# Kernel tuning notes

Hardware: AMD Instinct MI355X
Metric: run time of the kernel (lower is better)

## Reference

```python
import jax, jax.numpy as jnp
import numpy as np

B, NAV, H, W = 16, 36, 120, 160
HID, AEMB, NF = 512, 32, 4

def _conv(x, w, b, stride, pad, dil, groups):
    y = jax.lax.conv_general_dilated(x, w, stride, pad, rhs_dilation=dil, feature_group_count=groups)
    return y + b[None, :, None, None]

def _avgpool(x, k, s):
    y = jax.lax.reduce_window(x, 0.0, jax.lax.add, (1, 1) + k, (1, 1) + s, 'VALID')
    return y / float(k[0] * k[1])

def _conv2_block(x, w1, b1, w2, b2):
    # conv2_1: k5 stride (5,7) dilation 10 -> avgpool 3/3 -> conv2_2: k3 stride 2 dilation (1,2) -> avgpool (3,9)/3
    y = _conv(x, w1, b1, (5, 7), ((0, 0), (0, 0)), (10, 10), 1)
    y = _avgpool(y, (3, 3), (3, 3))
    y = _conv(y, w2, b2, (2, 2), ((0, 0), (0, 0)), (1, 2), 1)
    y = _avgpool(y, (3, 9), (3, 3))
    return y[:, 0]  # [B,3,12]

def setup_inputs() -> dict:
    key = jax.random.key(0)
    ks = jax.random.split(key, 24)
    s = 0.02
    d = {}
    d['depth_feat_0'] = jax.random.normal(ks[0], (B, NAV, H, W), jnp.float32)
    d['depth_feat_1'] = jax.random.normal(ks[1], (B, NAV, H, W), jnp.float32)
    d['obj_detection_feat'] = jax.random.normal(ks[2], (B, NAV, H, W), jnp.float32)
    d['num_navigable_feat'] = jax.random.uniform(ks[3], (B, NAV), jnp.float32)
    d['pre_action_feat'] = jax.random.normal(ks[4], (B, AEMB), jnp.float32)
    d['h_0'] = jax.random.normal(ks[5], (B, HID), jnp.float32)
    d['c_0'] = jax.random.normal(ks[6], (B, HID), jnp.float32)
    d['weighted_ctx'] = jax.random.normal(ks[7], (B, HID), jnp.float32)
    d['navigable_index'] = jax.random.randint(ks[8], (B, 8), 0, NAV).astype(jnp.int32)
    # params
    d['conv1_w'] = jax.random.normal(ks[9], (NAV, 2, 5, 5), jnp.float32) * s
    d['conv1_b'] = jnp.zeros((NAV,), jnp.float32)
    d['dyn_filters'] = jax.random.normal(ks[10], (NF, NAV, 2, 5, 5), jnp.float32) * s
    d['dyn_w1'] = jax.random.normal(ks[11], (HID, HID // 4), jnp.float32) * s
    d['dyn_b1'] = jnp.zeros((HID // 4,), jnp.float32)
    d['dyn_w2'] = jax.random.normal(ks[12], (HID // 4, NF), jnp.float32) * s
    d['dyn_b2'] = jnp.zeros((NF,), jnp.float32)
    d['conv2_1_w'] = jax.random.normal(ks[13], (1, 1, 5, 5), jnp.float32) * s
    d['conv2_1_b'] = jnp.zeros((1,), jnp.float32)
    d['conv2_2_w'] = jax.random.normal(ks[14], (1, 1, 3, 3), jnp.float32) * s
    d['conv2_2_b'] = jnp.zeros((1,), jnp.float32)
    in_sz = HID + NAV + NF + AEMB  # 584
    d['lstm_w_ih'] = jax.random.normal(ks[15], (4 * HID, in_sz), jnp.float32) * s
    d['lstm_w_hh'] = jax.random.normal(ks[16], (4 * HID, HID), jnp.float32) * s
    d['lstm_b_ih'] = jnp.zeros((4 * HID,), jnp.float32)
    d['lstm_b_hh'] = jnp.zeros((4 * HID,), jnp.float32)
    return d

def reference(depth_feat_0, depth_feat_1, obj_detection_feat, num_navigable_feat, pre_action_feat, h_0, c_0, weighted_ctx, navigable_index, conv1_w, conv1_b, dyn_filters, dyn_w1, dyn_b1, dyn_w2, dyn_b2, conv2_1_w, conv2_1_b, conv2_2_w, conv2_2_b, lstm_w_ih, lstm_w_hh, lstm_b_ih, lstm_b_hh):
    Bv = depth_feat_0.shape[0]
    # interleave depth channels: [B,72,H,W] (replaces 36-iter python copy loop)
    mid1 = jnp.stack([depth_feat_0, depth_feat_1], axis=2).reshape(Bv, 2 * NAV, H, W)
    total_depth = _conv(mid1, conv1_w, conv1_b, (1, 1), ((2, 2), (2, 2)), (1, 1), NAV)  # [B,36,H,W]
    nav_attn = jax.nn.softmax(num_navigable_feat, axis=1)[:, :, None, None]
    mid2 = jnp.stack([total_depth * nav_attn, obj_detection_feat * nav_attn], axis=2).reshape(Bv, 2 * NAV, H, W)
    # dynamic conv: per-sample filter = attention-weighted mix of NF learned grouped filters
    filt_attn = jax.nn.softmax(jax.nn.relu(weighted_ctx @ dyn_w1 + dyn_b1) @ dyn_w2 + dyn_b2, axis=1)  # [B,4]
    kern = jnp.einsum('bf,fgikl->bgikl', filt_attn, dyn_filters).reshape(Bv * NAV, 2, 5, 5)
    dyn_out = jax.lax.conv_general_dilated(mid2.reshape(1, Bv * 2 * NAV, H, W), kern, (1, 1), ((2, 2), (2, 2)), feature_group_count=Bv * NAV).reshape(Bv, NAV, H, W)
    # panorama canvas assembly: tile i -> row block (2 - i//12), col i%12
    canvas = dyn_out.reshape(Bv, 3, 12, H, W)[:, ::-1].transpose(0, 1, 3, 2, 4).reshape(Bv, 1, 3 * H, 12 * W)
    v1 = _conv2_block(canvas, conv2_1_w, conv2_1_b, conv2_2_w, conv2_2_b)
    rolled = jnp.concatenate([canvas[..., -W:], canvas[..., :-W]], axis=-1)
    v2 = _conv2_block(rolled, conv2_1_w, conv2_1_b, conv2_2_w, conv2_2_b)
    v2 = jnp.concatenate([v2[:, :, 1:], v2[:, :, :1]], axis=-1)
    vf = ((v1 + v2) * 0.5)[:, ::-1].reshape(Bv, NAV)  # flip row dim then flatten
    vf = jax.nn.softmax(vf / 10.0, axis=1)  # self.softmax_temperature hardcoded to 10
    concat = jnp.concatenate([weighted_ctx, vf, filt_attn, pre_action_feat], axis=1)
    gates = concat @ lstm_w_ih.T + lstm_b_ih + h_0 @ lstm_w_hh.T + lstm_b_hh
    i, f, g, o = jnp.split(gates, 4, axis=1)
    c_1 = jax.nn.sigmoid(f) * c_0 + jax.nn.sigmoid(i) * jnp.tanh(g)
    h_1 = jax.nn.sigmoid(o) * jnp.tanh(c_1)
    mask = jnp.zeros((Bv, NAV + 1), jnp.float32).at[:, 0].set(1.0)
    mask = mask.at[jnp.arange(Bv)[:, None], navigable_index + 1].set(1.0)
    return (h_1, c_1, vf, mask)
```

## Files before the change

### kernel.cpp

```cpp
#include <hip/hip_runtime.h>
#include <math.h>

#define B_ 16
#define NAV_ 36
#define H_ 120
#define W_ 160
#define HID_ 512
#define PLANES (B_*NAV_)
#define PLANE_PX (H_*W_)
#define CANVAS_H 360
#define CANVAS_W 1920
#define CANVAS_PX (CANVAS_H*CANVAS_W)

#define OUT_H 12
#define ST_ROWS 16
#define ROWB 352
#define CHSTR (ST_ROWS*ROWB)

#define WS_NAV    0
#define WS_FATT   576
#define WS_KERN   640
#define WS_TD     29440
#define WS_CANVAS (WS_TD + PLANES*PLANE_PX)
#define WS_POOL1  (WS_CANVAS + B_*CANVAS_PX)
#define WS_VF     (WS_POOL1 + B_*2*19*89)

typedef unsigned int u32;
typedef _Float16 h2_t __attribute__((ext_vector_type(2)));
typedef float float4a __attribute__((ext_vector_type(4), aligned(4)));

__device__ __forceinline__ float sigmoidf_(float x) { return 1.f / (1.f + expf(-x)); }

__device__ __forceinline__ u32 pkh(float a, float b) {
    return __builtin_bit_cast(u32, __builtin_amdgcn_cvt_pkrtz(a, b));
}
__device__ __forceinline__ float dot2h(u32 a, u32 b, float c) {
#if __has_builtin(__builtin_amdgcn_fdot2)
    return __builtin_amdgcn_fdot2(__builtin_bit_cast(h2_t, a),
                                  __builtin_bit_cast(h2_t, b), c, false);
#else
    float r;
    asm("v_dot2_f32_f16 %0, %1, %2, %3" : "=v"(r) : "v"(a), "v"(b), "v"(c));
    return r;
#endif
}

__device__ __forceinline__ void stage2(unsigned char* lds, const float* s0,
                                       const float* s1, int r0, int tid)
{
    for (int i = tid; i < 2*ST_ROWS*44; i += 256) {
        const int ch  = i / (ST_ROWS*44);
        const int rem = i % (ST_ROWS*44);
        const int rr  = rem / 44;
        const int j   = rem % 44;
        const int gr  = r0 - 2 + rr;
        u32 lo = 0, hi = 0;
        if ((unsigned)gr < (unsigned)H_ && j <= 40) {
            const float* src = (ch ? s1 : s0) + gr*W_;
            if (j == 0) {
                hi = pkh(src[0], src[1]);
            } else if (j < 40) {
                const float4a v = *(const float4a*)(src + 4*j - 2);
                lo = pkh(v.x, v.y);  hi = pkh(v.z, v.w);
            } else {
                lo = pkh(src[158], src[159]);
            }
        }
        *(int2*)(lds + (size_t)ch*CHSTR + rr*ROWB + j*8) = make_int2((int)lo, (int)hi);
    }
}

__device__ __forceinline__ void conv8(const unsigned char* b0, const unsigned char* b1,
                                      const u32* ew, float* acc)
{
    #pragma unroll
    for (int ky = 0; ky < 5; ++ky) {
        const int off = ky*ROWB;
        int4 qa = *(const int4*)(b0 + off);
        int2 qb = *(const int2*)(b0 + off + 16);
        int4 ra = *(const int4*)(b1 + off);
        int2 rb = *(const int2*)(b1 + off + 16);
        u32 P[6] = {(u32)qa.x,(u32)qa.y,(u32)qa.z,(u32)qa.w,(u32)qb.x,(u32)qb.y};
        u32 Q[6] = {(u32)ra.x,(u32)ra.y,(u32)ra.z,(u32)ra.w,(u32)rb.x,(u32)rb.y};
        const u32 e0 = ew[ky*3+0], e1 = ew[ky*3+1], e2 = ew[ky*3+2];
        const u32 f0 = ew[15+ky*3+0], f1 = ew[15+ky*3+1], f2 = ew[15+ky*3+2];
        const u32 o0 = e0 << 16;
        const u32 o1 = __builtin_amdgcn_alignbit(e1, e0, 16);
        const u32 o2 = __builtin_amdgcn_alignbit(e2, e1, 16);
        const u32 g0 = f0 << 16;
        const u32 g1 = __builtin_amdgcn_alignbit(f1, f0, 16);
        const u32 g2 = __builtin_amdgcn_alignbit(f2, f1, 16);
        #pragma unroll
        for (int m = 0; m < 4; ++m) {
            acc[2*m]   = dot2h(e0, P[m], dot2h(e1, P[m+1], dot2h(e2, P[m+2], acc[2*m])));
            acc[2*m+1] = dot2h(o0, P[m], dot2h(o1, P[m+1], dot2h(o2, P[m+2], acc[2*m+1])));
            acc[2*m]   = dot2h(f0, Q[m], dot2h(f1, Q[m+1], dot2h(f2, Q[m+2], acc[2*m])));
            acc[2*m+1] = dot2h(g0, Q[m], dot2h(g1, Q[m+1], dot2h(g2, Q[m+2], acc[2*m+1])));
        }
    }
}

#define LOAD_EW(EW, SW)                                                        \
    {                                                                          \
        _Pragma("unroll")                                                      \
        for (int q = 0; q < 7; ++q) {                                          \
            int4 t = ((const int4*)(SW))[q];                                   \
            EW[4*q]=(u32)t.x; EW[4*q+1]=(u32)t.y; EW[4*q+2]=(u32)t.z; EW[4*q+3]=(u32)t.w; \
        }                                                                      \
        int2 t = ((const int2*)(SW))[14];                                      \
        EW[28]=(u32)t.x; EW[29]=(u32)t.y;                                      \
    }

__global__ __launch_bounds__(256)
void k_td(const float* __restrict__ d0, const float* __restrict__ d1,
          const float* __restrict__ conv1_w, const float* __restrict__ conv1_b,
          const float* __restrict__ wctx, const float* __restrict__ dw1,
          const float* __restrict__ db1, const float* __restrict__ dw2,
          const float* __restrict__ db2, const float* __restrict__ dynf,
          const float* __restrict__ numnav, float* __restrict__ ws)
{
    const int tid = threadIdx.x;
    const int plane = blockIdx.y;

    __shared__ __align__(16) unsigned char smem[2*CHSTR + 160];
    u32* swt2 = (u32*)(smem + 2*CHSTR);
    float* sextra = (float*)(swt2 + 32);

    if (blockIdx.x == 10) {
        if (plane % NAV_) return;
        const int b = plane / NAV_;
        float* sh   = (float*)smem;
        float* sred = sh + 128;
        float* nv   = sh + 136;
        float* nms  = sh + 172;
        if (tid < 128) {
            float acc = db1[tid];
            for (int k = 0; k < HID_; ++k) acc += wctx[b*HID_ + k] * dw1[k*128 + tid];
            sh[tid] = fmaxf(acc, 0.f);
        }
        __syncthreads();
        if (tid < 4) {
            float acc = db2[tid];
            for (int j = 0; j < 128; ++j) acc += sh[j] * dw2[j*4 + tid];
            sred[tid] = acc;
        }
        __syncthreads();
        if (tid == 0) {
            float m = fmaxf(fmaxf(sred[0], sred[1]), fmaxf(sred[2], sred[3]));
            float e0 = expf(sred[0]-m), e1 = expf(sred[1]-m), e2 = expf(sred[2]-m), e3 = expf(sred[3]-m);
            float s = e0+e1+e2+e3;
            sred[4] = e0/s; sred[5] = e1/s; sred[6] = e2/s; sred[7] = e3/s;
            ws[WS_FATT + b*4+0] = sred[4]; ws[WS_FATT + b*4+1] = sred[5];
            ws[WS_FATT + b*4+2] = sred[6]; ws[WS_FATT + b*4+3] = sred[7];
        }
        __syncthreads();
        {
            const float fa0 = sred[4], fa1 = sred[5], fa2 = sred[6], fa3 = sred[7];
            for (int e = tid; e < 1800; e += 256) {
                float v = fa0*dynf[e] + fa1*dynf[1800+e] + fa2*dynf[3600+e] + fa3*dynf[5400+e];
                ws[WS_KERN + b*1800 + e] = v;
            }
        }
        if (tid < 36) nv[tid] = numnav[b*NAV_ + tid];
        __syncthreads();
        if (tid == 0) {
            float m = nv[0];
            for (int i = 1; i < 36; ++i) m = fmaxf(m, nv[i]);
            float s = 0.f;
            for (int i = 0; i < 36; ++i) s += expf(nv[i]-m);
            nms[0] = m; nms[1] = s;
        }
        __syncthreads();
        if (tid < 36) ws[WS_NAV + b*NAV_ + tid] = expf(nv[tid]-nms[0]) / nms[1];
        return;
    }

    const int g = plane % NAV_;
    const int r0 = blockIdx.x * OUT_H;

    if (tid < 30) {
        const int ch = tid / 15, ky = (tid % 15) / 3, k = tid % 3;
        const float* wsrc = conv1_w + g*50 + ch*25 + ky*5;
        const float a0 = wsrc[2*k];
        const float a1 = (k < 2) ? wsrc[2*k+1] : 0.f;
        swt2[tid] = pkh(a0, a1);
    }
    if (tid == 30) sextra[0] = conv1_b[g];

    stage2(smem, d0 + (size_t)plane*PLANE_PX, d1 + (size_t)plane*PLANE_PX, r0, tid);
    __syncthreads();

    if (tid < 240) {
        const int yr = tid / 20, s = tid % 20;
        const unsigned char* b0 = smem + yr*ROWB + s*16;
        const unsigned char* b1 = b0 + CHSTR;
        float acc[8];
        #pragma unroll
        for (int p = 0; p < 8; ++p) acc[p] = 0.f;
        u32 ew[30];
        LOAD_EW(ew, swt2)
        conv8(b0, b1, ew, acc);
        const float bias = sextra[0];
        float* outp = ws + WS_TD + (size_t)plane*PLANE_PX + (r0+yr)*W_ + s*8;
        *(float4*)outp     = make_float4(acc[0]+bias, acc[1]+bias, acc[2]+bias, acc[3]+bias);
        *(float4*)(outp+4) = make_float4(acc[4]+bias, acc[5]+bias, acc[6]+bias, acc[7]+bias);
    }
}

__global__ __launch_bounds__(256)
void k_dyn(const float* __restrict__ obj, float* __restrict__ ws)
{
    const int tid = threadIdx.x;
    const int plane = blockIdx.y;
    const int b = plane / NAV_;
    const int g = plane % NAV_;
    const int r0 = blockIdx.x * OUT_H;

    __shared__ __align__(16) unsigned char smem[2*CHSTR + 160];
    u32* swt2 = (u32*)(smem + 2*CHSTR);
    float* sextra = (float*)(swt2 + 32);

    if (tid < 30) {
        const int ch = tid / 15, ky = (tid % 15) / 3, k = tid % 3;
        const float* wsrc = ws + WS_KERN + plane*50 + ch*25 + ky*5;
        const float a0 = wsrc[2*k];
        const float a1 = (k < 2) ? wsrc[2*k+1] : 0.f;
        swt2[tid] = pkh(a0, a1);
    }
    if (tid == 30) sextra[0] = ws[WS_NAV + plane];

    stage2(smem, ws + WS_TD + (size_t)plane*PLANE_PX,
           obj + (size_t)plane*PLANE_PX, r0, tid);
    __syncthreads();

    if (tid < 240) {
        const int yr = tid / 20, s = tid % 20;
        const unsigned char* b0 = smem + yr*ROWB + s*16;
        const unsigned char* b1 = b0 + CHSTR;
        float acc[8];
        #pragma unroll
        for (int p = 0; p < 8; ++p) acc[p] = 0.f;
        u32 ew[30];
        LOAD_EW(ew, swt2)
        conv8(b0, b1, ew, acc);
        const float a = sextra[0];
        const int rowblk = 2 - g/12;
        const int colblk = g % 12;
        float* cbase = ws + WS_CANVAS + (size_t)b*CANVAS_PX
                     + (size_t)(rowblk*H_ + r0 + yr)*CANVAS_W + colblk*W_ + s*8;
        *(float4*)cbase     = make_float4(a*acc[0], a*acc[1], a*acc[2], a*acc[3]);
        *(float4*)(cbase+4) = make_float4(a*acc[4], a*acc[5], a*acc[6], a*acc[7]);
    }
}

__global__ __launch_bounds__(256)
void k_conv2a(const float* __restrict__ w21p, const float* __restrict__ b21p,
              float* __restrict__ ws)
{
    const int blk = blockIdx.x;
    const int a = blk % 19;
    const int bv = blk / 19;
    const int ver = bv & 1;
    const int b = bv >> 1;
    const int coloff = ver ? (CANVAS_W - W_) : 0;

    __shared__ float s1[3*267];
    __shared__ float swt[25];
    if (threadIdx.x < 25) swt[threadIdx.x] = w21p[threadIdx.x];
    __syncthreads();
    const float b21 = b21p[0];
    const float* cv = ws + WS_CANVAS + (size_t)b*CANVAS_PX;

    for (int px = threadIdx.x; px < 3*267; px += 256) {
        const int row = px / 267;
        const int v = px % 267;
        const int u = 3*a + row;
        float acc = b21;
        #pragma unroll
        for (int ky = 0; ky < 5; ++ky) {
            const float* rp = cv + (5*u + 10*ky)*CANVAS_W;
            #pragma unroll
            for (int kx = 0; kx < 5; ++kx) {
                int c = 7*v + 10*kx + coloff;
                if (c >= CANVAS_W) c -= CANVAS_W;
                acc += swt[ky*5+kx] * rp[c];
            }
        }
        s1[px] = acc;
    }
    __syncthreads();
    if (threadIdx.x < 89) {
        const int bb = threadIdx.x;
        float s = 0.f;
        #pragma unroll
        for (int i = 0; i < 3; ++i)
            #pragma unroll
            for (int j = 0; j < 3; ++j)
                s += s1[i*267 + 3*bb + j];
        ws[WS_POOL1 + blk*89 + bb] = s * (1.f/9.f);
    }
}

__global__ __launch_bounds__(256)
void k_conv2b(const float* __restrict__ w22p, const float* __restrict__ b22p,
              const int* __restrict__ navidx, float* __restrict__ ws,
              float* __restrict__ out)
{
    const int b = blockIdx.x;
    __shared__ float p[2*19*89];
    __shared__ float s2[2*9*43];
    __shared__ float svf[36];
    __shared__ float sms[2];
    __shared__ float swt[9];

    for (int i = threadIdx.x; i < 2*19*89; i += 256)
        p[i] = ws[WS_POOL1 + (b*2)*19*89 + i];
    if (threadIdx.x < 9) swt[threadIdx.x] = w22p[threadIdx.x];
    const float b22 = b22p[0];
    __syncthreads();

    for (int t = threadIdx.x; t < 2*9*43; t += 256) {
        const int ver = t / 387;
        const int r = t % 387;
        const int pp = r / 43;
        const int q = r % 43;
        float acc = b22;
        #pragma unroll
        for (int i = 0; i < 3; ++i)
            #pragma unroll
            for (int j = 0; j < 3; ++j)
                acc += swt[i*3+j] * p[(ver*19 + (2*pp+i))*89 + 2*q + 2*j];
        s2[ver*387 + pp*43 + q] = acc;
    }
    __syncthreads();

    if (threadIdx.x < 36) {
        const int gg = threadIdx.x;
        const int io = 2 - gg/12;
        const int j  = gg % 12;
        const int j2 = (j + 1) % 12;
        float s = 0.f;
        #pragma unroll
        for (int ii = 0; ii < 3; ++ii)
            #pragma unroll
            for (int jj = 0; jj < 9; ++jj)
                s += s2[(3*io+ii)*43 + 3*j + jj] + s2[387 + (3*io+ii)*43 + 3*j2 + jj];
        svf[gg] = s * (0.5f/27.f);
    }
    __syncthreads();
    if (threadIdx.x == 0) {
        float m = svf[0];
        for (int i = 1; i < 36; ++i) m = fmaxf(m, svf[i]);
        float s = 0.f;
        for (int i = 0; i < 36; ++i) s += expf((svf[i]-m)*0.1f);
        sms[0] = m; sms[1] = s;
    }
    __syncthreads();
    if (threadIdx.x < 36) {
        const float v = expf((svf[threadIdx.x]-sms[0])*0.1f) / sms[1];
        ws[WS_VF + b*36 + threadIdx.x] = v;
        out[16384 + b*36 + threadIdx.x] = v;
    }
    if (threadIdx.x < 37) {
        const int j = threadIdx.x;
        float v = (j == 0) ? 1.f : 0.f;
        #pragma unroll
        for (int t = 0; t < 8; ++t)
            if (navidx[b*8+t] + 1 == j) v = 1.f;
        out[16960 + b*37 + j] = v;
    }
}

#define CT_STRIDE 20
__global__ __launch_bounds__(256)
void k_lstm(const float* __restrict__ wctx, const float* __restrict__ pre_action,
            const float* __restrict__ h0, const float* __restrict__ c0,
            const float* __restrict__ w_ih, const float* __restrict__ w_hh,
            const float* __restrict__ b_ih, const float* __restrict__ b_hh,
            const float* __restrict__ ws, float* __restrict__ out)
{
    __shared__ float cT[1096*CT_STRIDE];
    __shared__ float red[8*32*16];
    __shared__ float gatev[8][16];
    const int tid = threadIdx.x;

    for (int idx = tid; idx < 1096*16; idx += 256) {
        const int k = idx >> 4;
        const int bb = idx & 15;
        float v;
        if (k < 512)       v = wctx[bb*512 + k];
        else if (k < 548)  v = ws[WS_VF + bb*36 + (k-512)];
        else if (k < 552)  v = ws[WS_FATT + bb*4 + (k-548)];
        else if (k < 584)  v = pre_action[bb*32 + (k-552)];
        else               v = h0[bb*512 + (k-584)];
        cT[k*CT_STRIDE + bb] = v;
    }
    __syncthreads();

    const int rl = tid >> 5;
    const int lane = tid & 31;
    const int u0 = blockIdx.x*2;
    const int ul = rl & 1;
    const int gate = rl >> 1;
    const int r = u0 + ul + gate*512;

    float acc[16];
    #pragma unroll
    for (int i = 0; i < 16; ++i) acc[i] = 0.f;

    const float* wih_r = w_ih + (size_t)r*584;
    for (int k = lane; k < 584; k += 32) {
        const float wv = wih_r[k];
        const float* cp = cT + k*CT_STRIDE;
        #pragma unroll
        for (int i = 0; i < 16; ++i) acc[i] += wv*cp[i];
    }
    const float* whh_r = w_hh + (size_t)r*512;
    for (int k = lane; k < 512; k += 32) {
        const float wv = whh_r[k];
        const float* cp = cT + (584+k)*CT_STRIDE;
        #pragma unroll
        for (int i = 0; i < 16; ++i) acc[i] += wv*cp[i];
    }
    float* rp = red + (rl*32 + lane)*16;
    #pragma unroll
    for (int i = 0; i < 16; ++i) rp[i] = acc[i];
    __syncthreads();

    if (tid < 128) {
        const int rr = tid >> 4;
        const int bb = tid & 15;
        const int rrow = u0 + (rr & 1) + (rr >> 1)*512;
        float s = b_ih[rrow] + b_hh[rrow];
        for (int l = 0; l < 32; ++l) s += red[(rr*32 + l)*16 + bb];
        gatev[rr][bb] = s;
    }
    __syncthreads();

    if (tid < 32) {
        const int ul2 = tid >> 4;
        const int bb = tid & 15;
        const int u = u0 + ul2;
        const float gi = gatev[0+ul2][bb];
        const float gf = gatev[2+ul2][bb];
        const float gg = gatev[4+ul2][bb];
        const float go = gatev[6+ul2][bb];
        const float c1 = sigmoidf_(gf)*c0[bb*512+u] + sigmoidf_(gi)*tanhf(gg);
        const float h1 = sigmoidf_(go)*tanhf(c1);
        out[bb*512 + u] = h1;
        out[8192 + bb*512 + u] = c1;
    }
}

extern "C" void kernel_launch(void* const* d_in, const int* in_sizes, int n_in,
                              void* d_out, int out_size, void* d_ws, size_t ws_size,
                              hipStream_t stream)
{
    const float* d0        = (const float*)d_in[0];
    const float* d1        = (const float*)d_in[1];
    const float* obj       = (const float*)d_in[2];
    const float* numnav    = (const float*)d_in[3];
    const float* preact    = (const float*)d_in[4];
    const float* h0        = (const float*)d_in[5];
    const float* c0        = (const float*)d_in[6];
    const float* wctx      = (const float*)d_in[7];
    const int*   navidx    = (const int*)d_in[8];
    const float* conv1_w   = (const float*)d_in[9];
    const float* conv1_b   = (const float*)d_in[10];
    const float* dynf      = (const float*)d_in[11];
    const float* dw1       = (const float*)d_in[12];
    const float* db1       = (const float*)d_in[13];
    const float* dw2       = (const float*)d_in[14];
    const float* db2       = (const float*)d_in[15];
    const float* w21       = (const float*)d_in[16];
    const float* b21       = (const float*)d_in[17];
    const float* w22       = (const float*)d_in[18];
    const float* b22       = (const float*)d_in[19];
    const float* wih       = (const float*)d_in[20];
    const float* whh       = (const float*)d_in[21];
    const float* bih       = (const float*)d_in[22];
    const float* bhh       = (const float*)d_in[23];
    float* ws  = (float*)d_ws;
    float* out = (float*)d_out;

    dim3 blk(256);
    k_td    <<<dim3(11, 576), blk, 0, stream>>>(d0, d1, conv1_w, conv1_b, wctx,
                                                dw1, db1, dw2, db2, dynf, numnav, ws);
    k_dyn   <<<dim3(10, 576), blk, 0, stream>>>(obj, ws);
    k_conv2a<<<dim3(608),     blk, 0, stream>>>(w21, b21, ws);
    k_conv2b<<<dim3(16),      blk, 0, stream>>>(w22, b22, navidx, ws, out);
    k_lstm  <<<dim3(256),     blk, 0, stream>>>(wctx, preact, h0, c0, wih, whh,
                                                bih, bhh, ws, out);
}
```

Before: 146.0 us.

## Fuse depth conv and dynamic conv into one kernel with halo recompute in LDS

```diff
diff --git a/kernel.cpp b/kernel.cpp
--- a/kernel.cpp
+++ b/kernel.cpp
@@ -13,9 +13,11 @@
 #define CANVAS_PX (CANVAS_H*CANVAS_W)
 
 #define OUT_H 12
-#define ST_ROWS 16
+#define IN_ROWS 20
+#define TD_ROWS 16
+#define OBJ_ROWS 16
 #define ROWB 352
-#define CHSTR (ST_ROWS*ROWB)
+#define INCH (IN_ROWS*ROWB)
 
 #define WS_NAV    0
 #define WS_FATT   576
@@ -43,31 +45,6 @@
     asm("v_dot2_f32_f16 %0, %1, %2, %3" : "=v"(r) : "v"(a), "v"(b), "v"(c));
     return r;
 #endif
-}
-
-__device__ __forceinline__ void stage2(unsigned char* lds, const float* s0,
-                                       const float* s1, int r0, int tid)
-{
-    for (int i = tid; i < 2*ST_ROWS*44; i += 256) {
-        const int ch  = i / (ST_ROWS*44);
-        const int rem = i % (ST_ROWS*44);
-        const int rr  = rem / 44;
-        const int j   = rem % 44;
-        const int gr  = r0 - 2 + rr;
-        u32 lo = 0, hi = 0;
-        if ((unsigned)gr < (unsigned)H_ && j <= 40) {
-            const float* src = (ch ? s1 : s0) + gr*W_;
-            if (j == 0) {
-                hi = pkh(src[0], src[1]);
-            } else if (j < 40) {
-                const float4a v = *(const float4a*)(src + 4*j - 2);
-                lo = pkh(v.x, v.y);  hi = pkh(v.z, v.w);
-            } else {
-                lo = pkh(src[158], src[159]);
-            }
-        }
-        *(int2*)(lds + (size_t)ch*CHSTR + rr*ROWB + j*8) = make_int2((int)lo, (int)hi);
-    }
 }
 
 __device__ __forceinline__ void conv8(const unsigned char* b0, const unsigned char* b1,
@@ -104,146 +81,164 @@
     {                                                                          \
         _Pragma("unroll")                                                      \
         for (int q = 0; q < 7; ++q) {                                          \
-            int4 t = ((const int4*)(SW))[q];                                   \
-            EW[4*q]=(u32)t.x; EW[4*q+1]=(u32)t.y; EW[4*q+2]=(u32)t.z; EW[4*q+3]=(u32)t.w; \
+            int4 t_ = ((const int4*)(SW))[q];                                  \
+            EW[4*q]=(u32)t_.x; EW[4*q+1]=(u32)t_.y; EW[4*q+2]=(u32)t_.z; EW[4*q+3]=(u32)t_.w; \
         }                                                                      \
-        int2 t = ((const int2*)(SW))[14];                                      \
-        EW[28]=(u32)t.x; EW[29]=(u32)t.y;                                      \
+        int2 t_ = ((const int2*)(SW))[14];                                     \
+        EW[28]=(u32)t_.x; EW[29]=(u32)t_.y;                                    \
     }
 
 __global__ __launch_bounds__(256)
-void k_td(const float* __restrict__ d0, const float* __restrict__ d1,
-          const float* __restrict__ conv1_w, const float* __restrict__ conv1_b,
-          const float* __restrict__ wctx, const float* __restrict__ dw1,
-          const float* __restrict__ db1, const float* __restrict__ dw2,
-          const float* __restrict__ db2, const float* __restrict__ dynf,
-          const float* __restrict__ numnav, float* __restrict__ ws)
+void k_pre(const float* __restrict__ wctx, const float* __restrict__ dw1,
+           const float* __restrict__ db1, const float* __restrict__ dw2,
+           const float* __restrict__ db2, const float* __restrict__ dynf,
+           const float* __restrict__ numnav, float* __restrict__ ws)
 {
     const int tid = threadIdx.x;
-    const int plane = blockIdx.y;
-
-    __shared__ __align__(16) unsigned char smem[2*CHSTR + 160];
-    u32* swt2 = (u32*)(smem + 2*CHSTR);
-    float* sextra = (float*)(swt2 + 32);
-
-    if (blockIdx.x == 10) {
-        if (plane % NAV_) return;
-        const int b = plane / NAV_;
-        float* sh   = (float*)smem;
-        float* sred = sh + 128;
-        float* nv   = sh + 136;
-        float* nms  = sh + 172;
-        if (tid < 128) {
-            float acc = db1[tid];
-            for (int k = 0; k < HID_; ++k) acc += wctx[b*HID_ + k] * dw1[k*128 + tid];
-            sh[tid] = fmaxf(acc, 0.f);
-        }
-        __syncthreads();
-        if (tid < 4) {
-            float acc = db2[tid];
-            for (int j = 0; j < 128; ++j) acc += sh[j] * dw2[j*4 + tid];
-            sred[tid] = acc;
-        }
-        __syncthreads();
-        if (tid == 0) {
-            float m = fmaxf(fmaxf(sred[0], sred[1]), fmaxf(sred[2], sred[3]));
-            float e0 = expf(sred[0]-m), e1 = expf(sred[1]-m), e2 = expf(sred[2]-m), e3 = expf(sred[3]-m);
-            float s = e0+e1+e2+e3;
-            sred[4] = e0/s; sred[5] = e1/s; sred[6] = e2/s; sred[7] = e3/s;
-            ws[WS_FATT + b*4+0] = sred[4]; ws[WS_FATT + b*4+1] = sred[5];
-            ws[WS_FATT + b*4+2] = sred[6]; ws[WS_FATT + b*4+3] = sred[7];
-        }
-        __syncthreads();
-        {
-            const float fa0 = sred[4], fa1 = sred[5], fa2 = sred[6], fa3 = sred[7];
-            for (int e = tid; e < 1800; e += 256) {
-                float v = fa0*dynf[e] + fa1*dynf[1800+e] + fa2*dynf[3600+e] + fa3*dynf[5400+e];
-                ws[WS_KERN + b*1800 + e] = v;
-            }
-        }
-        if (tid < 36) nv[tid] = numnav[b*NAV_ + tid];
-        __syncthreads();
-        if (tid == 0) {
-            float m = nv[0];
-            for (int i = 1; i < 36; ++i) m = fmaxf(m, nv[i]);
-            float s = 0.f;
-            for (int i = 0; i < 36; ++i) s += expf(nv[i]-m);
-            nms[0] = m; nms[1] = s;
-        }
-        __syncthreads();
-        if (tid < 36) ws[WS_NAV + b*NAV_ + tid] = expf(nv[tid]-nms[0]) / nms[1];
-        return;
-    }
-
-    const int g = plane % NAV_;
-    const int r0 = blockIdx.x * OUT_H;
-
-    if (tid < 30) {
-        const int ch = tid / 15, ky = (tid % 15) / 3, k = tid % 3;
-        const float* wsrc = conv1_w + g*50 + ch*25 + ky*5;
-        const float a0 = wsrc[2*k];
-        const float a1 = (k < 2) ? wsrc[2*k+1] : 0.f;
-        swt2[tid] = pkh(a0, a1);
-    }
-    if (tid == 30) sextra[0] = conv1_b[g];
-
-    stage2(smem, d0 + (size_t)plane*PLANE_PX, d1 + (size_t)plane*PLANE_PX, r0, tid);
-    __syncthreads();
-
-    if (tid < 240) {
-        const int yr = tid / 20, s = tid % 20;
-        const unsigned char* b0 = smem + yr*ROWB + s*16;
-        const unsigned char* b1 = b0 + CHSTR;
-        float acc[8];
-        #pragma unroll
-        for (int p = 0; p < 8; ++p) acc[p] = 0.f;
-        u32 ew[30];
-        LOAD_EW(ew, swt2)
-        conv8(b0, b1, ew, acc);
-        const float bias = sextra[0];
-        float* outp = ws + WS_TD + (size_t)plane*PLANE_PX + (r0+yr)*W_ + s*8;
-        *(float4*)outp     = make_float4(acc[0]+bias, acc[1]+bias, acc[2]+bias, acc[3]+bias);
-        *(float4*)(outp+4) = make_float4(acc[4]+bias, acc[5]+bias, acc[6]+bias, acc[7]+bias);
-    }
+    const int b = blockIdx.x;
+    __shared__ float sh[128];
+    __shared__ float sred[8];
+    __shared__ float nv[36];
+    __shared__ float nms[2];
+    if (tid < 128) {
+        float acc = db1[tid];
+        for (int k = 0; k < HID_; ++k) acc += wctx[b*HID_ + k] * dw1[k*128 + tid];
+        sh[tid] = fmaxf(acc, 0.f);
+    }
+    __syncthreads();
+    if (tid < 4) {
+        float acc = db2[tid];
+        for (int j = 0; j < 128; ++j) acc += sh[j] * dw2[j*4 + tid];
+        sred[tid] = acc;
+    }
+    __syncthreads();
+    if (tid == 0) {
+        float m = fmaxf(fmaxf(sred[0], sred[1]), fmaxf(sred[2], sred[3]));
+        float e0 = expf(sred[0]-m), e1 = expf(sred[1]-m), e2 = expf(sred[2]-m), e3 = expf(sred[3]-m);
+        float s = e0+e1+e2+e3;
+        sred[4] = e0/s; sred[5] = e1/s; sred[6] = e2/s; sred[7] = e3/s;
+        ws[WS_FATT + b*4+0] = sred[4]; ws[WS_FATT + b*4+1] = sred[5];
+        ws[WS_FATT + b*4+2] = sred[6]; ws[WS_FATT + b*4+3] = sred[7];
+    }
+    __syncthreads();
+    {
+        const float fa0 = sred[4], fa1 = sred[5], fa2 = sred[6], fa3 = sred[7];
+        for (int e = tid; e < 1800; e += 256) {
+            float v = fa0*dynf[e] + fa1*dynf[1800+e] + fa2*dynf[3600+e] + fa3*dynf[5400+e];
+            ws[WS_KERN + b*1800 + e] = v;
+        }
+    }
+    if (tid < 36) nv[tid] = numnav[b*NAV_ + tid];
+    __syncthreads();
+    if (tid == 0) {
+        float m = nv[0];
+        for (int i = 1; i < 36; ++i) m = fmaxf(m, nv[i]);
+        float s = 0.f;
+        for (int i = 0; i < 36; ++i) s += expf(nv[i]-m);
+        nms[0] = m; nms[1] = s;
+    }
+    __syncthreads();
+    if (tid < 36) ws[WS_NAV + b*NAV_ + tid] = expf(nv[tid]-nms[0]) / nms[1];
 }
 
 __global__ __launch_bounds__(256)
-void k_dyn(const float* __restrict__ obj, float* __restrict__ ws)
+void k_fused(const float* __restrict__ d0, const float* __restrict__ d1,
+             const float* __restrict__ obj, const float* __restrict__ conv1_w,
+             const float* __restrict__ conv1_b, float* __restrict__ ws)
 {
     const int tid = threadIdx.x;
+    const int band = blockIdx.x;
     const int plane = blockIdx.y;
     const int b = plane / NAV_;
     const int g = plane % NAV_;
-    const int r0 = blockIdx.x * OUT_H;
-
-    __shared__ __align__(16) unsigned char smem[2*CHSTR + 160];
-    u32* swt2 = (u32*)(smem + 2*CHSTR);
-    float* sextra = (float*)(swt2 + 32);
+    const int r0 = band * OUT_H;
+
+    __shared__ __align__(16) unsigned char smem[2*INCH + OBJ_ROWS*ROWB + TD_ROWS*ROWB + 256];
+    unsigned char* inL  = smem;
+    unsigned char* objL = smem + 2*INCH;
+    unsigned char* tdL  = objL + OBJ_ROWS*ROWB;
+    u32* wts = (u32*)(tdL + TD_ROWS*ROWB);
 
     if (tid < 30) {
-        const int ch = tid / 15, ky = (tid % 15) / 3, k = tid % 3;
+        const int ch = tid/15, ky = (tid%15)/3, k = tid%3;
+        const float* wsrc = conv1_w + g*50 + ch*25 + ky*5;
+        wts[tid] = pkh(wsrc[2*k], (k < 2) ? wsrc[2*k+1] : 0.f);
+    } else if (tid >= 32 && tid < 62) {
+        const int t2 = tid - 32;
+        const int ch = t2/15, ky = (t2%15)/3, k = t2%3;
         const float* wsrc = ws + WS_KERN + plane*50 + ch*25 + ky*5;
-        const float a0 = wsrc[2*k];
-        const float a1 = (k < 2) ? wsrc[2*k+1] : 0.f;
-        swt2[tid] = pkh(a0, a1);
-    }
-    if (tid == 30) sextra[0] = ws[WS_NAV + plane];
-
-    stage2(smem, ws + WS_TD + (size_t)plane*PLANE_PX,
-           obj + (size_t)plane*PLANE_PX, r0, tid);
-    __syncthreads();
-
-    if (tid < 240) {
-        const int yr = tid / 20, s = tid % 20;
-        const unsigned char* b0 = smem + yr*ROWB + s*16;
-        const unsigned char* b1 = b0 + CHSTR;
+        wts[tid] = pkh(wsrc[2*k], (k < 2) ? wsrc[2*k+1] : 0.f);
+    } else if (tid == 62) ((float*)wts)[62] = conv1_b[g];
+    else if (tid == 63)   ((float*)wts)[63] = ws[WS_NAV + plane];
+
+    const float* pd0 = d0 + (size_t)plane*PLANE_PX;
+    const float* pd1 = d1 + (size_t)plane*PLANE_PX;
+    const float* pob = obj + (size_t)plane*PLANE_PX;
+    for (int i = tid; i < 2*IN_ROWS*44 + OBJ_ROWS*44; i += 256) {
+        const float* src; unsigned char* dst; int row, j, gr;
+        if (i < 2*IN_ROWS*44) {
+            const int ch = i/(IN_ROWS*44), rem = i%(IN_ROWS*44);
+            row = rem/44; j = rem%44; gr = r0 - 4 + row;
+            src = ch ? pd1 : pd0;
+            dst = inL + (size_t)ch*INCH + row*ROWB + j*8;
+        } else {
+            const int k = i - 2*IN_ROWS*44;
+            row = k/44; j = k%44; gr = r0 - 2 + row;
+            src = pob;
+            dst = objL + row*ROWB + j*8;
+        }
+        u32 lo = 0, hi = 0;
+        if ((unsigned)gr < (unsigned)H_ && j <= 40) {
+            const float* sp = src + gr*W_;
+            if (j == 0) hi = pkh(sp[0], sp[1]);
+            else if (j < 40) { const float4a v = *(const float4a*)(sp + 4*j - 2);
+                               lo = pkh(v.x, v.y);  hi = pkh(v.z, v.w); }
+            else lo = pkh(sp[158], sp[159]);
+        }
+        *(int2*)dst = make_int2((int)lo, (int)hi);
+    }
+    if (tid < 32) {
+        const int rr = tid >> 1;
+        *(u32*)(tdL + rr*ROWB + ((tid & 1) ? 324 : 0)) = 0;
+    }
+    __syncthreads();
+
+    for (int t = tid; t < TD_ROWS*20; t += 256) {
+        const int tr = t/20, s = t%20;
+        const int gr = r0 - 2 + tr;
+        u32* rowp = (u32*)(tdL + tr*ROWB);
+        if ((unsigned)gr >= (unsigned)H_) {
+            rowp[4*s+1] = 0;
+            *(int2*)(rowp + 4*s + 2) = make_int2(0, 0);
+            rowp[4*s+4] = 0;
+            continue;
+        }
         float acc[8];
         #pragma unroll
         for (int p = 0; p < 8; ++p) acc[p] = 0.f;
         u32 ew[30];
-        LOAD_EW(ew, swt2)
-        conv8(b0, b1, ew, acc);
-        const float a = sextra[0];
+        LOAD_EW(ew, wts)
+        conv8(inL + tr*ROWB + s*16, inL + INCH + tr*ROWB + s*16, ew, acc);
+        const float bias = ((const float*)wts)[62];
+        const u32 p0 = pkh(acc[0]+bias, acc[1]+bias);
+        const u32 p1 = pkh(acc[2]+bias, acc[3]+bias);
+        const u32 p2 = pkh(acc[4]+bias, acc[5]+bias);
+        const u32 p3 = pkh(acc[6]+bias, acc[7]+bias);
+        rowp[4*s+1] = p0;
+        *(int2*)(rowp + 4*s + 2) = make_int2((int)p1, (int)p2);
+        rowp[4*s+4] = p3;
+    }
+    __syncthreads();
+
+    if (tid < OUT_H*20) {
+        const int yr = tid/20, s = tid%20;
+        float acc[8];
+        #pragma unroll
+        for (int p = 0; p < 8; ++p) acc[p] = 0.f;
+        u32 ew[30];
+        LOAD_EW(ew, wts + 32)
+        conv8(tdL + yr*ROWB + s*16, objL + yr*ROWB + s*16, ew, acc);
+        const float a = ((const float*)wts)[63];
         const int rowblk = 2 - g/12;
         const int colblk = g % 12;
         float* cbase = ws + WS_CANVAS + (size_t)b*CANVAS_PX
@@ -484,9 +479,8 @@
     float* out = (float*)d_out;
 
     dim3 blk(256);
-    k_td    <<<dim3(11, 576), blk, 0, stream>>>(d0, d1, conv1_w, conv1_b, wctx,
-                                                dw1, db1, dw2, db2, dynf, numnav, ws);
-    k_dyn   <<<dim3(10, 576), blk, 0, stream>>>(obj, ws);
+    k_pre   <<<dim3(16),      blk, 0, stream>>>(wctx, dw1, db1, dw2, db2, dynf, numnav, ws);
+    k_fused <<<dim3(10, 576), blk, 0, stream>>>(d0, d1, obj, conv1_w, conv1_b, ws);
     k_conv2a<<<dim3(608),     blk, 0, stream>>>(w21, b21, ws);
     k_conv2b<<<dim3(16),      blk, 0, stream>>>(w22, b22, navidx, ws, out);
     k_lstm  <<<dim3(256),     blk, 0, stream>>>(wctx, preact, h0, c0, wih, whh,
```

Result: slower. 159.6 us (+9.4%).
